# Performance work log

Hardware: AMD Instinct MI355X
Metric: run time of the kernel (lower is better)

Reference implementation:

```python
import jax, jax.numpy as jnp
import numpy as np

B, S, D, H = 2, 2048, 1024, 16
HD = D // H               # head_dim = input_size / num_heads
STEPS = 1                 # update_steps_max extra Hopfield update steps
LN_EPS = 1e-5
SCALING = 1.0 / np.sqrt(HD)  # beta = 1/sqrt(head_dim)


def layernorm(x, g, b):
    m = x.mean(-1, keepdims=True)
    v = ((x - m) ** 2).mean(-1, keepdims=True)
    return (x - m) * jax.lax.rsqrt(v + LN_EPS) * g + b


def setup_inputs() -> dict:
    key = jax.random.key(0)
    ks = jax.random.split(key, 9)
    s = 0.02
    f32 = jnp.float32
    return {
        "data": jax.random.normal(ks[0], (B, S, D), f32),
        # affine LayerNorm params (stored / state / projection patterns)
        "g_k": jnp.ones((D,), f32), "b_k": jnp.zeros((D,), f32),
        "g_q": jnp.ones((D,), f32), "b_q": jnp.zeros((D,), f32),
        "g_v": jnp.ones((D,), f32), "b_v": jnp.zeros((D,), f32),
        # in-projections (q/k/v) and out-projection of HopfieldCore
        "Wq": jax.random.normal(ks[1], (D, D), f32) * s, "bq": jnp.zeros((D,), f32),
        "Wk": jax.random.normal(ks[2], (D, D), f32) * s, "bk": jnp.zeros((D,), f32),
        "Wv": jax.random.normal(ks[3], (D, D), f32) * s, "bv": jnp.zeros((D,), f32),
        "Wo": jax.random.normal(ks[4], (D, D), f32) * s, "bo": jnp.zeros((D,), f32),
    }


def reference(data, g_k, b_k, g_q, b_q, g_v, b_v,
              Wq, bq, Wk, bk, Wv, bv, Wo, bo):
    # single input tensor used as stored / state / projection pattern
    xk = layernorm(data, g_k, b_k)   # stored pattern  -> keys
    xq = layernorm(data, g_q, b_q)   # state pattern   -> queries
    xv = layernorm(data, g_v, b_v)   # pattern proj    -> values

    split = lambda t: t.reshape(B, S, H, HD).transpose(0, 2, 1, 3)  # [B,H,S,HD]
    q = split(xq @ Wq + bq)
    k = split(xk @ Wk + bk)
    v = split(xv @ Wv + bv)

    def assoc(q):  # xi = softmax(beta * q K^T)
        return jax.nn.softmax(
            jnp.einsum('bhqd,bhkd->bhqk', q, k) * SCALING, axis=-1)

    xi = assoc(q)
    for _ in range(STEPS):           # iterative Hopfield update: q <- xi K
        q = jnp.einsum('bhqk,bhkd->bhqd', xi, k)
        xi = assoc(q)

    out = jnp.einsum('bhqk,bhkd->bhqd', xi, v)        # retrieve with values
    out = out.transpose(0, 2, 1, 3).reshape(B, S, D)  # merge heads
    return out @ Wo + bo
```

## Files before the change

kernel.cpp:

```cpp
#include <hip/hip_runtime.h>
#include <hip/hip_bf16.h>

#define B_  2
#define S_  2048
#define D_  1024
#define H_  16
#define HD_ 64
#define M_  4096


typedef __attribute__((ext_vector_type(8))) short short8;
typedef __attribute__((ext_vector_type(4))) float f32x4;

#define CE_ 0.1803368801111204f
#define SD_ 56

static __device__ __forceinline__ unsigned short f2bfc(float f){
  union{float f; unsigned u;} c; c.f = f;
  return (unsigned short)((c.u + 0x8000u) >> 16);
}
static __device__ __forceinline__ unsigned pk2bf(float a, float b){
  union{float f; unsigned u;} ca, cb; ca.f=a; cb.f=b;
  return __builtin_amdgcn_perm(cb.u + 0x8000u, ca.u + 0x8000u, 0x07060302u);
}
static __device__ __forceinline__ unsigned pk2bft(float a, float b){
  union{float f; unsigned u;} ca, cb; ca.f=a; cb.f=b;
  return __builtin_amdgcn_perm(cb.u, ca.u, 0x07060302u);
}

__global__ __launch_bounds__(256) void stats_kernel(const float* __restrict__ x,
                                                    float* __restrict__ mean,
                                                    float* __restrict__ rstd){
  int row = blockIdx.x*4 + (threadIdx.x>>6);
  int l = threadIdx.x & 63;
  const float4* xr = (const float4*)(x + (size_t)row*D_);
  float s = 0.f, ss = 0.f;
  #pragma unroll
  for (int i=0;i<4;i++){
    float4 v = xr[l + 64*i];
    s  += v.x+v.y+v.z+v.w;
    ss += v.x*v.x+v.y*v.y+v.z*v.z+v.w*v.w;
  }
  #pragma unroll
  for (int m=1;m<64;m<<=1){ s += __shfl_xor(s, m, 64); ss += __shfl_xor(ss, m, 64); }
  if (l==0){
    float me = s*(1.0f/D_);
    float var = ss*(1.0f/D_) - me*me;
    mean[row] = me;
    rstd[row] = rsqrtf(var + 1e-5f);
  }
}

__global__ __launch_bounds__(256) void biasfold_kernel(
  const float* __restrict__ Wq, const float* __restrict__ Wk, const float* __restrict__ Wv,
  const float* __restrict__ blq, const float* __restrict__ blk, const float* __restrict__ blv,
  const float* __restrict__ bpq, const float* __restrict__ bpk, const float* __restrict__ bpv,
  float* __restrict__ bf){
  int z = blockIdx.y;
  const float* W  = (z==0)?Wq:(z==1)?Wk:Wv;
  const float* bl = (z==0)?blq:(z==1)?blk:blv;
  const float* bp = (z==0)?bpq:(z==1)?bpk:bpv;
  int nl = threadIdx.x & 63, kg = threadIdx.x >> 6;
  int n = blockIdx.x*64 + nl;
  float acc = 0.f;
  for (int k = kg*256; k < (kg+1)*256; k++)
    acc += bl[k] * W[(size_t)k*D_ + n];
  __shared__ float red[4][64];
  red[kg][nl] = acc;
  __syncthreads();
  if (threadIdx.x < 64){
    int nn = blockIdx.x*64 + threadIdx.x;
    float v = red[0][threadIdx.x]+red[1][threadIdx.x]+red[2][threadIdx.x]+red[3][threadIdx.x]
              + bp[nn];
    bf[z*D_ + nn] = (z==0) ? v*CE_ : v;
  }
}

__global__ __launch_bounds__(256) void wtrans_kernel(
  const float* __restrict__ Wq, const float* __restrict__ Wk,
  const float* __restrict__ Wv, const float* __restrict__ Wo,
  const float* __restrict__ gq, const float* __restrict__ gk,
  const float* __restrict__ gv,
  unsigned short* __restrict__ WT){
  int z = blockIdx.z;
  const float* W = (z==0)?Wq:(z==1)?Wk:(z==2)?Wv:Wo;
  const float* g = (z==0)?gq:(z==1)?gk:(z==2)?gv:(const float*)0;
  unsigned short* out = WT + ((size_t)z<<20);
  int k0 = blockIdx.x*64, n0 = blockIdx.y*64;
  __shared__ unsigned short tile[64][72];
  int t = threadIdx.x;
  {
    int kr = t>>2, c16 = (t&3)*16;
    float gs = g ? g[k0+kr]*((z==0)?CE_:1.0f) : 1.0f;
    const float* src = W + (size_t)(k0+kr)*D_ + n0 + c16;
    float4 w0 = *(const float4*)(src);
    float4 w1 = *(const float4*)(src+4);
    float4 w2 = *(const float4*)(src+8);
    float4 w3 = *(const float4*)(src+12);
    unsigned* tp = (unsigned*)&tile[kr][c16];
    tp[0]=pk2bf(w0.x*gs,w0.y*gs); tp[1]=pk2bf(w0.z*gs,w0.w*gs);
    tp[2]=pk2bf(w1.x*gs,w1.y*gs); tp[3]=pk2bf(w1.z*gs,w1.w*gs);
    tp[4]=pk2bf(w2.x*gs,w2.y*gs); tp[5]=pk2bf(w2.z*gs,w2.w*gs);
    tp[6]=pk2bf(w3.x*gs,w3.y*gs); tp[7]=pk2bf(w3.z*gs,w3.w*gs);
  }
  __syncthreads();
  {
    int nr = t>>2, kc = (t&3)*16;
    union { uint4 v[2]; unsigned short u[16]; } st;
    #pragma unroll
    for (int i=0;i<16;i++) st.u[i] = tile[kc+i][nr];
    unsigned short* dst = out + (size_t)(n0+nr)*D_ + k0 + kc;
    *(uint4*)(dst)     = st.v[0];
    *(uint4*)(dst + 8) = st.v[1];
  }
}

__global__ __launch_bounds__(256) void gemm_qkv(
  const float* __restrict__ data,
  const unsigned short* __restrict__ WT,
  const float* __restrict__ biasf,
  const float* __restrict__ mean, const float* __restrict__ rstd,
  unsigned short* __restrict__ qv, unsigned short* __restrict__ kb,
  unsigned short* __restrict__ kT, unsigned short* __restrict__ vT)
{
  int z = blockIdx.z;
  const unsigned short* Bt = WT + ((size_t)z<<20);
  const float* bias = biasf + z*D_;
  unsigned short* oN = (z==0)?qv:(z==1)?kb:(unsigned short*)0;
  unsigned short* oT = (z==0)?(unsigned short*)0:(z==1)?kT:vT;

  __shared__ __align__(16) unsigned short As[128*SD_];
  __shared__ __align__(16) unsigned short Bs[128*SD_];
  int tid = threadIdx.x, w = tid>>6, l = tid&63;
  int m0 = blockIdx.x*128, n0 = blockIdx.y*128;
  int wr = (w>>1)*64, wc = (w&1)*64;
  int lr = l&15, qd = l>>4;
  int srow = tid>>2, scol = (tid&3)*8;

  float rs0 = rstd[m0+srow],    nm0 = -mean[m0+srow]*rs0;
  float rs1 = rstd[m0+srow+64], nm1 = -mean[m0+srow+64]*rs1;

  const f32x4 fz = {0.f,0.f,0.f,0.f};
  f32x4 acc[4][4];
  #pragma unroll
  for (int i=0;i<4;i++)
    #pragma unroll
    for (int j=0;j<4;j++) acc[i][j] = fz;

  for (int kk=0; kk<D_; kk+=32){
    __syncthreads();
    {
      const float* p0 = data + (size_t)(m0+srow   )*D_ + kk + scol;
      const float* p1 = data + (size_t)(m0+srow+64)*D_ + kk + scol;
      float4 a0 = *(const float4*)(p0), a0b = *(const float4*)(p0+4);
      float4 a1 = *(const float4*)(p1), a1b = *(const float4*)(p1+4);
      uint4 o0, o1;
      o0.x = pk2bf(fmaf(a0.x ,rs0,nm0), fmaf(a0.y ,rs0,nm0));
      o0.y = pk2bf(fmaf(a0.z ,rs0,nm0), fmaf(a0.w ,rs0,nm0));
      o0.z = pk2bf(fmaf(a0b.x,rs0,nm0), fmaf(a0b.y,rs0,nm0));
      o0.w = pk2bf(fmaf(a0b.z,rs0,nm0), fmaf(a0b.w,rs0,nm0));
      o1.x = pk2bf(fmaf(a1.x ,rs1,nm1), fmaf(a1.y ,rs1,nm1));
      o1.y = pk2bf(fmaf(a1.z ,rs1,nm1), fmaf(a1.w ,rs1,nm1));
      o1.z = pk2bf(fmaf(a1b.x,rs1,nm1), fmaf(a1b.y,rs1,nm1));
      o1.w = pk2bf(fmaf(a1b.z,rs1,nm1), fmaf(a1b.w,rs1,nm1));
      *(uint4*)(As + srow*SD_      + scol) = o0;
      *(uint4*)(As + (srow+64)*SD_ + scol) = o1;
    }
    *(uint4*)(Bs + srow*SD_      + scol) = *(const uint4*)(Bt + (size_t)(n0+srow   )*D_ + kk + scol);
    *(uint4*)(Bs + (srow+64)*SD_ + scol) = *(const uint4*)(Bt + (size_t)(n0+srow+64)*D_ + kk + scol);
    __syncthreads();
    short8 af[4], bfr[4];
    #pragma unroll
    for (int i=0;i<4;i++) af[i]  = *(const short8*)(As + (wr + i*16 + lr)*SD_ + qd*8);
    #pragma unroll
    for (int j=0;j<4;j++) bfr[j] = *(const short8*)(Bs + (wc + j*16 + lr)*SD_ + qd*8);
    #pragma unroll
    for (int i=0;i<4;i++)
      #pragma unroll
      for (int j=0;j<4;j++)
        acc[i][j] = __builtin_amdgcn_mfma_f32_16x16x32_bf16(af[i], bfr[j], acc[i][j], 0, 0, 0);
  }

  #pragma unroll
  for (int j=0;j<4;j++){
    int n = n0 + wc + j*16 + lr;
    float bias_n = bias[n];
    #pragma unroll
    for (int i=0;i<4;i++){
      int mb = m0 + wr + i*16 + qd*4;
      float v0 = acc[i][j][0] + bias_n;
      float v1 = acc[i][j][1] + bias_n;
      float v2 = acc[i][j][2] + bias_n;
      float v3 = acc[i][j][3] + bias_n;
      if (oN){
        oN[(size_t)(mb+0)*D_ + n] = f2bfc(v0);
        oN[(size_t)(mb+1)*D_ + n] = f2bfc(v1);
        oN[(size_t)(mb+2)*D_ + n] = f2bfc(v2);
        oN[(size_t)(mb+3)*D_ + n] = f2bfc(v3);
      }
      if (oT){
        int bb = mb >> 11, sI = mb & (S_-1);
        int hh = n >> 6,  dd = n & 63;
        uint2 pk; pk.x = pk2bf(v0, v1); pk.y = pk2bf(v2, v3);
        *(uint2*)(oT + (size_t)((bb*H_ + hh)*HD_ + dd)*S_ + sI) = pk;
      }
    }
  }
}

__global__ __launch_bounds__(256) void gemm_out(
  const unsigned short* __restrict__ A,
  const unsigned short* __restrict__ Bt,
  const float* __restrict__ bo,
  float* __restrict__ Cf)
{
  __shared__ __align__(16) unsigned short As[128*SD_];
  __shared__ __align__(16) unsigned short Bs[128*SD_];
  int tid = threadIdx.x, w = tid>>6, l = tid&63;
  int m0 = blockIdx.x*128, n0 = blockIdx.y*128;
  int wr = (w>>1)*64, wc = (w&1)*64;
  int lr = l&15, qd = l>>4;
  int srow = tid>>2, scol = (tid&3)*8;

  const f32x4 fz = {0.f,0.f,0.f,0.f};
  f32x4 acc[4][4];
  #pragma unroll
  for (int i=0;i<4;i++)
    #pragma unroll
    for (int j=0;j<4;j++) acc[i][j] = fz;

  for (int kk=0; kk<D_; kk+=32){
    __syncthreads();
    *(uint4*)(As + srow*SD_      + scol) = *(const uint4*)(A  + (size_t)(m0+srow   )*D_ + kk + scol);
    *(uint4*)(As + (srow+64)*SD_ + scol) = *(const uint4*)(A  + (size_t)(m0+srow+64)*D_ + kk + scol);
    *(uint4*)(Bs + srow*SD_      + scol) = *(const uint4*)(Bt + (size_t)(n0+srow   )*D_ + kk + scol);
    *(uint4*)(Bs + (srow+64)*SD_ + scol) = *(const uint4*)(Bt + (size_t)(n0+srow+64)*D_ + kk + scol);
    __syncthreads();
    short8 af[4], bfr[4];
    #pragma unroll
    for (int i=0;i<4;i++) af[i]  = *(const short8*)(As + (wr + i*16 + lr)*SD_ + qd*8);
    #pragma unroll
    for (int j=0;j<4;j++) bfr[j] = *(const short8*)(Bs + (wc + j*16 + lr)*SD_ + qd*8);
    #pragma unroll
    for (int i=0;i<4;i++)
      #pragma unroll
      for (int j=0;j<4;j++)
        acc[i][j] = __builtin_amdgcn_mfma_f32_16x16x32_bf16(af[i], bfr[j], acc[i][j], 0, 0, 0);
  }

  #pragma unroll
  for (int j=0;j<4;j++){
    int n = n0 + wc + j*16 + lr;
    float bias_n = bo[n];
    #pragma unroll
    for (int i=0;i<4;i++){
      int mb = m0 + wr + i*16 + qd*4;
      Cf[(size_t)(mb+0)*D_ + n] = acc[i][j][0] + bias_n;
      Cf[(size_t)(mb+1)*D_ + n] = acc[i][j][1] + bias_n;
      Cf[(size_t)(mb+2)*D_ + n] = acc[i][j][2] + bias_n;
      Cf[(size_t)(mb+3)*D_ + n] = acc[i][j][3] + bias_n;
    }
  }
}

__global__ __launch_bounds__(256) void attn_fused(
  unsigned short* __restrict__ QO,
  const unsigned short* __restrict__ K,
  const unsigned short* __restrict__ KT,
  const unsigned short* __restrict__ VT)
{
  int qt = blockIdx.x;
  int h  = blockIdx.y;
  int b  = qt >> 4;
  int bh = b*H_ + h;
  int tid = threadIdx.x, w = tid>>6, l = tid&63;
  int lr = l&15, qd = l>>4;
  int r8 = tid>>3, c8 = (tid&7)*8;
  int chf = c8>>5, co = c8&31;

  __shared__ __align__(16) unsigned short sK[2][64*SD_];
  __shared__ __align__(16) unsigned short sV[2][64*SD_];
  __shared__ __align__(16) unsigned short sP[4][2][32*SD_];

  const f32x4 fz = {0.f,0.f,0.f,0.f};

  unsigned short* Qbase = QO + (size_t)(qt*128 + w*32) * D_ + h*64;
  short8 qf[2][2];
  #pragma unroll
  for (int gg=0; gg<2; gg++)
    #pragma unroll
    for (int hf=0; hf<2; hf++)
      qf[gg][hf] = *(const short8*)(Qbase + (size_t)(gg*16+lr)*D_ + hf*32 + qd*8);

  const unsigned short* Khead = K + (size_t)(b*S_)*D_ + h*64;
  const unsigned short* Vh0 = KT + (size_t)bh*HD_*S_;
  const unsigned short* Vh1 = VT + (size_t)bh*HD_*S_;
  unsigned short* Pw0 = &sP[w][0][0];
  unsigned short* Pw1 = &sP[w][1][0];

  f32x4 oacc[2][4];
  float lac[2];

  uint4 kr0, kr1, vr0, vr1;
  {
    kr0 = *(const uint4*)(Khead + (size_t)(r8   )*D_ + c8);
    kr1 = *(const uint4*)(Khead + (size_t)(r8+32)*D_ + c8);
    vr0 = *(const uint4*)(Vh0 + (size_t)(r8   )*S_ + c8);
    vr1 = *(const uint4*)(Vh0 + (size_t)(r8+32)*S_ + c8);
  }

  #pragma unroll 1
  for (int phase=0; phase<2; phase++){
    const unsigned short* Vhead = phase ? Vh1 : Vh0;
    lac[0]=0.f; lac[1]=0.f;
    #pragma unroll
    for (int gg=0;gg<2;gg++)
      #pragma unroll
      for (int t=0;t<4;t++) oacc[gg][t]=fz;

    for (int kt=0; kt<S_; kt+=64){
      __syncthreads();
      *(uint4*)(&sK[chf][(r8   )*SD_ + co]) = kr0;
      *(uint4*)(&sK[chf][(r8+32)*SD_ + co]) = kr1;
      *(uint4*)(&sV[chf][(r8   )*SD_ + co]) = vr0;
      *(uint4*)(&sV[chf][(r8+32)*SD_ + co]) = vr1;
      __syncthreads();

      {
        int nkt = kt + 64;
        const unsigned short* Vn = Vhead;
        if (nkt >= S_){ nkt = 0; Vn = Vh1; }
        kr0 = *(const uint4*)(Khead + (size_t)(nkt+r8   )*D_ + c8);
        kr1 = *(const uint4*)(Khead + (size_t)(nkt+r8+32)*D_ + c8);
        vr0 = *(const uint4*)(Vn + (size_t)(r8   )*S_ + nkt + c8);
        vr1 = *(const uint4*)(Vn + (size_t)(r8+32)*S_ + nkt + c8);
      }

      f32x4 sc[2][4];
      #pragma unroll
      for (int st=0; st<4; st++){
        short8 kA0 = *(const short8*)(&sK[0][(st*16+lr)*SD_ + qd*8]);
        short8 kA1 = *(const short8*)(&sK[1][(st*16+lr)*SD_ + qd*8]);
        #pragma unroll
        for (int gg=0; gg<2; gg++){
          f32x4 z = fz;
          z = __builtin_amdgcn_mfma_f32_16x16x32_bf16(kA0, qf[gg][0], z, 0,0,0);
          z = __builtin_amdgcn_mfma_f32_16x16x32_bf16(kA1, qf[gg][1], z, 0,0,0);
          sc[gg][st] = z;
        }
      }
      #pragma unroll
      for (int gg=0; gg<2; gg++)
        #pragma unroll
        for (int st=0; st<4; st++){
          float p0=__builtin_amdgcn_exp2f(sc[gg][st][0]);
          float p1=__builtin_amdgcn_exp2f(sc[gg][st][1]);
          float p2=__builtin_amdgcn_exp2f(sc[gg][st][2]);
          float p3=__builtin_amdgcn_exp2f(sc[gg][st][3]);
          lac[gg] += (p0+p1)+(p2+p3);
          uint2 pk; pk.x = pk2bft(p0,p1); pk.y = pk2bft(p2,p3);
          unsigned short* Ph = (st&2) ? Pw1 : Pw0;
          *(uint2*)(Ph + (gg*16+lr)*SD_ + (st&1)*16 + qd*4) = pk;
        }
      short8 pf[2][2];
      #pragma unroll
      for (int gg=0; gg<2; gg++){
        pf[gg][0] = *(const short8*)(Pw0 + (gg*16+lr)*SD_ + qd*8);
        pf[gg][1] = *(const short8*)(Pw1 + (gg*16+lr)*SD_ + qd*8);
      }
      #pragma unroll
      for (int dt=0; dt<4; dt++){
        short8 vA0 = *(const short8*)(&sV[0][(dt*16+lr)*SD_ + qd*8]);
        short8 vA1 = *(const short8*)(&sV[1][(dt*16+lr)*SD_ + qd*8]);
        #pragma unroll
        for (int gg=0; gg<2; gg++){
          oacc[gg][dt] = __builtin_amdgcn_mfma_f32_16x16x32_bf16(vA0, pf[gg][0], oacc[gg][dt], 0,0,0);
          oacc[gg][dt] = __builtin_amdgcn_mfma_f32_16x16x32_bf16(vA1, pf[gg][1], oacc[gg][dt], 0,0,0);
        }
      }
    }

    #pragma unroll
    for (int gg=0;gg<2;gg++){
      lac[gg] += __shfl_xor(lac[gg], 16, 64);
      lac[gg] += __shfl_xor(lac[gg], 32, 64);
    }

    if (phase==0){
      #pragma unroll
      for (int gg=0;gg<2;gg++){
        float iv = CE_ * __builtin_amdgcn_rcpf(lac[gg]);
        #pragma unroll
        for (int dt=0;dt<4;dt++){
          uint2 pk;
          pk.x = pk2bf(oacc[gg][dt][0]*iv, oacc[gg][dt][1]*iv);
          pk.y = pk2bf(oacc[gg][dt][2]*iv, oacc[gg][dt][3]*iv);
          unsigned short* Ph = (dt&2) ? Pw1 : Pw0;
          *(uint2*)(Ph + (gg*16+lr)*SD_ + (dt&1)*16 + qd*4) = pk;
        }
      }
      __builtin_amdgcn_s_waitcnt(0);
      #pragma unroll
      for (int gg=0;gg<2;gg++){
        qf[gg][0] = *(const short8*)(Pw0 + (gg*16+lr)*SD_ + qd*8);
        qf[gg][1] = *(const short8*)(Pw1 + (gg*16+lr)*SD_ + qd*8);
      }
    } else {
      #pragma unroll
      for (int gg=0;gg<2;gg++){
        float iv = __builtin_amdgcn_rcpf(lac[gg]);
        unsigned short* Ob = QO + (size_t)(qt*128 + w*32 + gg*16 + lr)*D_ + h*64;
        #pragma unroll
        for (int dt=0;dt<4;dt++){
          uint2 pk;
          pk.x = pk2bf(oacc[gg][dt][0]*iv, oacc[gg][dt][1]*iv);
          pk.y = pk2bf(oacc[gg][dt][2]*iv, oacc[gg][dt][3]*iv);
          *(uint2*)(Ob + dt*16 + qd*4) = pk;
        }
      }
    }
  }
}

extern "C" void kernel_launch(void* const* d_in, const int* in_sizes, int n_in,
                              void* d_out, int out_size, void* d_ws, size_t ws_size,
                              hipStream_t stream){
  const float* data = (const float*)d_in[0];
  const float* g_k  = (const float*)d_in[1];
  const float* b_k  = (const float*)d_in[2];
  const float* g_q  = (const float*)d_in[3];
  const float* b_q  = (const float*)d_in[4];
  const float* g_v  = (const float*)d_in[5];
  const float* b_v  = (const float*)d_in[6];
  const float* Wq   = (const float*)d_in[7];
  const float* bq   = (const float*)d_in[8];
  const float* Wk   = (const float*)d_in[9];
  const float* bk   = (const float*)d_in[10];
  const float* Wv   = (const float*)d_in[11];
  const float* bv   = (const float*)d_in[12];
  const float* Wo   = (const float*)d_in[13];
  const float* bo   = (const float*)d_in[14];
  float* out = (float*)d_out;

  char* ws = (char*)d_ws;
  const size_t MB = (size_t)1<<20;
  unsigned short* q    = (unsigned short*)(ws);
  unsigned short* kb   = (unsigned short*)(ws + 8*MB);
  unsigned short* WT   = (unsigned short*)(ws + 16*MB);
  unsigned short* WTo  = WT + ((size_t)3<<20);
  float*          bfld = (float*)(ws + 24*MB);
  float*          mean = bfld + 3*D_;
  float*          rstd = mean + M_;
  unsigned short* vT   = (unsigned short*)d_out;
  unsigned short* kT   = (unsigned short*)((char*)d_out + 8*MB);

  dim3 gb(256);
  stats_kernel<<<dim3(M_/4), gb, 0, stream>>>(data, mean, rstd);
  biasfold_kernel<<<dim3(16,3), gb, 0, stream>>>(Wq,Wk,Wv, b_q,b_k,b_v, bq,bk,bv, bfld);
  wtrans_kernel<<<dim3(16,16,4), gb, 0, stream>>>(Wq,Wk,Wv,Wo, g_q,g_k,g_v, WT);
  gemm_qkv<<<dim3(32,8,3), gb, 0, stream>>>(data, WT, bfld, mean, rstd, q, kb, kT, vT);
  attn_fused<<<dim3(32, H_), gb, 0, stream>>>(q, kb, kT, vT);
  gemm_out<<<dim3(32,8), gb, 0, stream>>>(q, WTo, bo, out);
}
```

Measured before the change: 292.4 us.

## Merge prep kernels, use direct global-to-LDS loads, widen attention key tiles

Folds the stats, bias-fold and weight-transpose kernels into one prep launch to cut launch overhead. Both GEMMs now stage their bf16 operand tiles with global_load_lds directly into unpadded LDS rows, skipping the register round trip. The attention kernel processes 128-key tiles in two 64-key sub-steps. It computes the softmax row sums with an MFMA against a ones vector instead of scalar adds plus cross-lane shuffles. The unpadded LDS rows risk bank conflicts, and the per-wave P buffer shrinks to 16 rows and is reused across query groups, which relies on in-order LDS access.

```diff
diff --git a/kernel.cpp b/kernel.cpp
--- a/kernel.cpp
+++ b/kernel.cpp
@@ -15,6 +15,12 @@
 #define CE_ 0.1803368801111204f
 #define SD_ 56
 
+typedef __attribute__((address_space(1))) const unsigned GU;
+typedef __attribute__((address_space(3))) unsigned LU;
+static __device__ __forceinline__ void glds16(const void* g, void* l){
+  __builtin_amdgcn_global_load_lds((GU*)g, (LU*)l, 16, 0, 0);
+}
+
 static __device__ __forceinline__ unsigned short f2bfc(float f){
   union{float f; unsigned u;} c; c.f = f;
   return (unsigned short)((c.u + 0x8000u) >> 16);
@@ -28,90 +34,86 @@
   return __builtin_amdgcn_perm(cb.u, ca.u, 0x07060302u);
 }
 
-__global__ __launch_bounds__(256) void stats_kernel(const float* __restrict__ x,
-                                                    float* __restrict__ mean,
-                                                    float* __restrict__ rstd){
-  int row = blockIdx.x*4 + (threadIdx.x>>6);
-  int l = threadIdx.x & 63;
-  const float4* xr = (const float4*)(x + (size_t)row*D_);
-  float s = 0.f, ss = 0.f;
-  #pragma unroll
-  for (int i=0;i<4;i++){
-    float4 v = xr[l + 64*i];
-    s  += v.x+v.y+v.z+v.w;
-    ss += v.x*v.x+v.y*v.y+v.z*v.z+v.w*v.w;
-  }
-  #pragma unroll
-  for (int m=1;m<64;m<<=1){ s += __shfl_xor(s, m, 64); ss += __shfl_xor(ss, m, 64); }
-  if (l==0){
-    float me = s*(1.0f/D_);
-    float var = ss*(1.0f/D_) - me*me;
-    mean[row] = me;
-    rstd[row] = rsqrtf(var + 1e-5f);
-  }
-}
-
-__global__ __launch_bounds__(256) void biasfold_kernel(
-  const float* __restrict__ Wq, const float* __restrict__ Wk, const float* __restrict__ Wv,
+__global__ __launch_bounds__(256) void prep_kernel(
+  const float* __restrict__ data, float* __restrict__ mean, float* __restrict__ rstd,
+  const float* __restrict__ Wq, const float* __restrict__ Wk,
+  const float* __restrict__ Wv, const float* __restrict__ Wo,
+  const float* __restrict__ gq, const float* __restrict__ gk, const float* __restrict__ gv,
   const float* __restrict__ blq, const float* __restrict__ blk, const float* __restrict__ blv,
   const float* __restrict__ bpq, const float* __restrict__ bpk, const float* __restrict__ bpv,
-  float* __restrict__ bf){
-  int z = blockIdx.y;
-  const float* W  = (z==0)?Wq:(z==1)?Wk:Wv;
-  const float* bl = (z==0)?blq:(z==1)?blk:blv;
-  const float* bp = (z==0)?bpq:(z==1)?bpk:bpv;
-  int nl = threadIdx.x & 63, kg = threadIdx.x >> 6;
-  int n = blockIdx.x*64 + nl;
-  float acc = 0.f;
-  for (int k = kg*256; k < (kg+1)*256; k++)
-    acc += bl[k] * W[(size_t)k*D_ + n];
+  unsigned short* __restrict__ WT, float* __restrict__ bf)
+{
+  __shared__ unsigned short tile[64][72];
   __shared__ float red[4][64];
-  red[kg][nl] = acc;
-  __syncthreads();
-  if (threadIdx.x < 64){
-    int nn = blockIdx.x*64 + threadIdx.x;
-    float v = red[0][threadIdx.x]+red[1][threadIdx.x]+red[2][threadIdx.x]+red[3][threadIdx.x]
-              + bp[nn];
-    bf[z*D_ + nn] = (z==0) ? v*CE_ : v;
-  }
-}
-
-__global__ __launch_bounds__(256) void wtrans_kernel(
-  const float* __restrict__ Wq, const float* __restrict__ Wk,
-  const float* __restrict__ Wv, const float* __restrict__ Wo,
-  const float* __restrict__ gq, const float* __restrict__ gk,
-  const float* __restrict__ gv,
-  unsigned short* __restrict__ WT){
-  int z = blockIdx.z;
-  const float* W = (z==0)?Wq:(z==1)?Wk:(z==2)?Wv:Wo;
-  const float* g = (z==0)?gq:(z==1)?gk:(z==2)?gv:(const float*)0;
-  unsigned short* out = WT + ((size_t)z<<20);
-  int k0 = blockIdx.x*64, n0 = blockIdx.y*64;
-  __shared__ unsigned short tile[64][72];
-  int t = threadIdx.x;
-  {
-    int kr = t>>2, c16 = (t&3)*16;
-    float gs = g ? g[k0+kr]*((z==0)?CE_:1.0f) : 1.0f;
-    const float* src = W + (size_t)(k0+kr)*D_ + n0 + c16;
-    float4 w0 = *(const float4*)(src);
-    float4 w1 = *(const float4*)(src+4);
-    float4 w2 = *(const float4*)(src+8);
-    float4 w3 = *(const float4*)(src+12);
-    unsigned* tp = (unsigned*)&tile[kr][c16];
-    tp[0]=pk2bf(w0.x*gs,w0.y*gs); tp[1]=pk2bf(w0.z*gs,w0.w*gs);
-    tp[2]=pk2bf(w1.x*gs,w1.y*gs); tp[3]=pk2bf(w1.z*gs,w1.w*gs);
-    tp[4]=pk2bf(w2.x*gs,w2.y*gs); tp[5]=pk2bf(w2.z*gs,w2.w*gs);
-    tp[6]=pk2bf(w3.x*gs,w3.y*gs); tp[7]=pk2bf(w3.z*gs,w3.w*gs);
-  }
-  __syncthreads();
-  {
-    int nr = t>>2, kc = (t&3)*16;
-    union { uint4 v[2]; unsigned short u[16]; } st;
-    #pragma unroll
-    for (int i=0;i<16;i++) st.u[i] = tile[kc+i][nr];
-    unsigned short* dst = out + (size_t)(n0+nr)*D_ + k0 + kc;
-    *(uint4*)(dst)     = st.v[0];
-    *(uint4*)(dst + 8) = st.v[1];
+  int bid = blockIdx.x, t = threadIdx.x;
+  if (bid < 1024){
+    int row = bid*4 + (t>>6);
+    int l = t & 63;
+    const float4* xr = (const float4*)(data + (size_t)row*D_);
+    float s = 0.f, ss = 0.f;
+    #pragma unroll
+    for (int i=0;i<4;i++){
+      float4 v = xr[l + 64*i];
+      s  += v.x+v.y+v.z+v.w;
+      ss += v.x*v.x+v.y*v.y+v.z*v.z+v.w*v.w;
+    }
+    #pragma unroll
+    for (int m=1;m<64;m<<=1){ s += __shfl_xor(s, m, 64); ss += __shfl_xor(ss, m, 64); }
+    if (l==0){
+      float me = s*(1.0f/D_);
+      float var = ss*(1.0f/D_) - me*me;
+      mean[row] = me;
+      rstd[row] = rsqrtf(var + 1e-5f);
+    }
+  } else if (bid < 2048){
+    int idx = bid - 1024;
+    int z = idx >> 8, rem = idx & 255;
+    int k0 = (rem>>4)*64, n0 = (rem&15)*64;
+    const float* W = (z==0)?Wq:(z==1)?Wk:(z==2)?Wv:Wo;
+    const float* g = (z==0)?gq:(z==1)?gk:(z==2)?gv:(const float*)0;
+    unsigned short* out = WT + ((size_t)z<<20);
+    {
+      int kr = t>>2, c16 = (t&3)*16;
+      float gs = g ? g[k0+kr]*((z==0)?CE_:1.0f) : 1.0f;
+      const float* src = W + (size_t)(k0+kr)*D_ + n0 + c16;
+      float4 w0 = *(const float4*)(src);
+      float4 w1 = *(const float4*)(src+4);
+      float4 w2 = *(const float4*)(src+8);
+      float4 w3 = *(const float4*)(src+12);
+      unsigned* tp = (unsigned*)&tile[kr][c16];
+      tp[0]=pk2bf(w0.x*gs,w0.y*gs); tp[1]=pk2bf(w0.z*gs,w0.w*gs);
+      tp[2]=pk2bf(w1.x*gs,w1.y*gs); tp[3]=pk2bf(w1.z*gs,w1.w*gs);
+      tp[4]=pk2bf(w2.x*gs,w2.y*gs); tp[5]=pk2bf(w2.z*gs,w2.w*gs);
+      tp[6]=pk2bf(w3.x*gs,w3.y*gs); tp[7]=pk2bf(w3.z*gs,w3.w*gs);
+    }
+    __syncthreads();
+    {
+      int nr = t>>2, kc = (t&3)*16;
+      union { uint4 v[2]; unsigned short u[16]; } st;
+      #pragma unroll
+      for (int i=0;i<16;i++) st.u[i] = tile[kc+i][nr];
+      unsigned short* dst = out + (size_t)(n0+nr)*D_ + k0 + kc;
+      *(uint4*)(dst)     = st.v[0];
+      *(uint4*)(dst + 8) = st.v[1];
+    }
+  } else {
+    int idx = bid - 2048;
+    int z = idx >> 4, xb = idx & 15;
+    const float* W  = (z==0)?Wq:(z==1)?Wk:Wv;
+    const float* bl = (z==0)?blq:(z==1)?blk:blv;
+    const float* bp = (z==0)?bpq:(z==1)?bpk:bpv;
+    int nl = t & 63, kg = t >> 6;
+    int n = xb*64 + nl;
+    float acc = 0.f;
+    for (int k = kg*256; k < (kg+1)*256; k++)
+      acc += bl[k] * W[(size_t)k*D_ + n];
+    red[kg][nl] = acc;
+    __syncthreads();
+    if (t < 64){
+      int nn = xb*64 + t;
+      float v = red[0][t]+red[1][t]+red[2][t]+red[3][t] + bp[nn];
+      bf[z*D_ + nn] = (z==0) ? v*CE_ : v;
+    }
   }
 }
 
@@ -130,7 +132,7 @@
   unsigned short* oT = (z==0)?(unsigned short*)0:(z==1)?kT:vT;
 
   __shared__ __align__(16) unsigned short As[128*SD_];
-  __shared__ __align__(16) unsigned short Bs[128*SD_];
+  __shared__ __align__(16) unsigned short Bs[128*32];
   int tid = threadIdx.x, w = tid>>6, l = tid&63;
   int m0 = blockIdx.x*128, n0 = blockIdx.y*128;
   int wr = (w>>1)*64, wc = (w&1)*64;
@@ -140,6 +142,10 @@
   float rs0 = rstd[m0+srow],    nm0 = -mean[m0+srow]*rs0;
   float rs1 = rstd[m0+srow+64], nm1 = -mean[m0+srow+64]*rs1;
 
+  const unsigned short* gB = Bt + (size_t)(n0 + w*32 + (l>>2))*D_ + (l&3)*8;
+  unsigned short* lB0 = &Bs[(w*32)*32];
+  unsigned short* lB1 = &Bs[(w*32+16)*32];
+
   const f32x4 fz = {0.f,0.f,0.f,0.f};
   f32x4 acc[4][4];
   #pragma unroll
@@ -149,6 +155,8 @@
 
   for (int kk=0; kk<D_; kk+=32){
     __syncthreads();
+    glds16(gB + kk,                lB0);
+    glds16(gB + kk + (size_t)16*D_, lB1);
     {
       const float* p0 = data + (size_t)(m0+srow   )*D_ + kk + scol;
       const float* p1 = data + (size_t)(m0+srow+64)*D_ + kk + scol;
@@ -166,14 +174,12 @@
       *(uint4*)(As + srow*SD_      + scol) = o0;
       *(uint4*)(As + (srow+64)*SD_ + scol) = o1;
     }
-    *(uint4*)(Bs + srow*SD_      + scol) = *(const uint4*)(Bt + (size_t)(n0+srow   )*D_ + kk + scol);
-    *(uint4*)(Bs + (srow+64)*SD_ + scol) = *(const uint4*)(Bt + (size_t)(n0+srow+64)*D_ + kk + scol);
     __syncthreads();
     short8 af[4], bfr[4];
     #pragma unroll
     for (int i=0;i<4;i++) af[i]  = *(const short8*)(As + (wr + i*16 + lr)*SD_ + qd*8);
     #pragma unroll
-    for (int j=0;j<4;j++) bfr[j] = *(const short8*)(Bs + (wc + j*16 + lr)*SD_ + qd*8);
+    for (int j=0;j<4;j++) bfr[j] = *(const short8*)(Bs + (wc + j*16 + lr)*32 + qd*8);
     #pragma unroll
     for (int i=0;i<4;i++)
       #pragma unroll
@@ -214,13 +220,19 @@
   const float* __restrict__ bo,
   float* __restrict__ Cf)
 {
-  __shared__ __align__(16) unsigned short As[128*SD_];
-  __shared__ __align__(16) unsigned short Bs[128*SD_];
+  __shared__ __align__(16) unsigned short As[128*32];
+  __shared__ __align__(16) unsigned short Bs[128*32];
   int tid = threadIdx.x, w = tid>>6, l = tid&63;
   int m0 = blockIdx.x*128, n0 = blockIdx.y*128;
   int wr = (w>>1)*64, wc = (w&1)*64;
   int lr = l&15, qd = l>>4;
-  int srow = tid>>2, scol = (tid&3)*8;
+
+  const unsigned short* gA = A  + (size_t)(m0 + w*32 + (l>>2))*D_ + (l&3)*8;
+  const unsigned short* gB = Bt + (size_t)(n0 + w*32 + (l>>2))*D_ + (l&3)*8;
+  unsigned short* lA0 = &As[(w*32)*32];
+  unsigned short* lA1 = &As[(w*32+16)*32];
+  unsigned short* lB0 = &Bs[(w*32)*32];
+  unsigned short* lB1 = &Bs[(w*32+16)*32];
 
   const f32x4 fz = {0.f,0.f,0.f,0.f};
   f32x4 acc[4][4];
@@ -231,16 +243,16 @@
 
   for (int kk=0; kk<D_; kk+=32){
     __syncthreads();
-    *(uint4*)(As + srow*SD_      + scol) = *(const uint4*)(A  + (size_t)(m0+srow   )*D_ + kk + scol);
-    *(uint4*)(As + (srow+64)*SD_ + scol) = *(const uint4*)(A  + (size_t)(m0+srow+64)*D_ + kk + scol);
-    *(uint4*)(Bs + srow*SD_      + scol) = *(const uint4*)(Bt + (size_t)(n0+srow   )*D_ + kk + scol);
-    *(uint4*)(Bs + (srow+64)*SD_ + scol) = *(const uint4*)(Bt + (size_t)(n0+srow+64)*D_ + kk + scol);
+    glds16(gA + kk,                 lA0);
+    glds16(gA + kk + (size_t)16*D_, lA1);
+    glds16(gB + kk,                 lB0);
+    glds16(gB + kk + (size_t)16*D_, lB1);
     __syncthreads();
     short8 af[4], bfr[4];
     #pragma unroll
-    for (int i=0;i<4;i++) af[i]  = *(const short8*)(As + (wr + i*16 + lr)*SD_ + qd*8);
-    #pragma unroll
-    for (int j=0;j<4;j++) bfr[j] = *(const short8*)(Bs + (wc + j*16 + lr)*SD_ + qd*8);
+    for (int i=0;i<4;i++) af[i]  = *(const short8*)(As + (wr + i*16 + lr)*32 + qd*8);
+    #pragma unroll
+    for (int j=0;j<4;j++) bfr[j] = *(const short8*)(Bs + (wc + j*16 + lr)*32 + qd*8);
     #pragma unroll
     for (int i=0;i<4;i++)
       #pragma unroll
@@ -269,20 +281,20 @@
   const unsigned short* __restrict__ KT,
   const unsigned short* __restrict__ VT)
 {
-  int qt = blockIdx.x;
-  int h  = blockIdx.y;
-  int b  = qt >> 4;
-  int bh = b*H_ + h;
+  int qt = blockIdx.x, h = blockIdx.y;
+  int b = qt >> 4, bh = b*H_ + h;
   int tid = threadIdx.x, w = tid>>6, l = tid&63;
   int lr = l&15, qd = l>>4;
   int r8 = tid>>3, c8 = (tid&7)*8;
   int chf = c8>>5, co = c8&31;
 
-  __shared__ __align__(16) unsigned short sK[2][64*SD_];
-  __shared__ __align__(16) unsigned short sV[2][64*SD_];
-  __shared__ __align__(16) unsigned short sP[4][2][32*SD_];
+  __shared__ __align__(16) unsigned short sK[2][128*SD_];
+  __shared__ __align__(16) unsigned short sV[4][64*SD_];
+  __shared__ __align__(16) unsigned short sP[4][2][16*SD_];
 
   const f32x4 fz = {0.f,0.f,0.f,0.f};
+  const short8 vones = {(short)0x3F80,(short)0x3F80,(short)0x3F80,(short)0x3F80,
+                        (short)0x3F80,(short)0x3F80,(short)0x3F80,(short)0x3F80};
 
   unsigned short* Qbase = QO + (size_t)(qt*128 + w*32) * D_ + h*64;
   short8 qf[2][2];
@@ -298,117 +310,116 @@
   unsigned short* Pw0 = &sP[w][0][0];
   unsigned short* Pw1 = &sP[w][1][0];
 
-  f32x4 oacc[2][4];
-  float lac[2];
-
-  uint4 kr0, kr1, vr0, vr1;
-  {
-    kr0 = *(const uint4*)(Khead + (size_t)(r8   )*D_ + c8);
-    kr1 = *(const uint4*)(Khead + (size_t)(r8+32)*D_ + c8);
-    vr0 = *(const uint4*)(Vh0 + (size_t)(r8   )*S_ + c8);
-    vr1 = *(const uint4*)(Vh0 + (size_t)(r8+32)*S_ + c8);
-  }
+  f32x4 oacc[2][4], sacc[2];
+
+  uint4 kr[4], vr[4];
+  #pragma unroll
+  for (int j=0;j<4;j++)
+    kr[j] = *(const uint4*)(Khead + (size_t)(r8 + j*32)*D_ + c8);
+  vr[0] = *(const uint4*)(Vh0 + (size_t)(r8   )*S_ + c8);
+  vr[1] = *(const uint4*)(Vh0 + (size_t)(r8+32)*S_ + c8);
+  vr[2] = *(const uint4*)(Vh0 + (size_t)(r8   )*S_ + 64 + c8);
+  vr[3] = *(const uint4*)(Vh0 + (size_t)(r8+32)*S_ + 64 + c8);
 
   #pragma unroll 1
   for (int phase=0; phase<2; phase++){
     const unsigned short* Vhead = phase ? Vh1 : Vh0;
-    lac[0]=0.f; lac[1]=0.f;
+    sacc[0]=fz; sacc[1]=fz;
     #pragma unroll
     for (int gg=0;gg<2;gg++)
       #pragma unroll
       for (int t=0;t<4;t++) oacc[gg][t]=fz;
 
-    for (int kt=0; kt<S_; kt+=64){
+    for (int kt=0; kt<S_; kt+=128){
       __syncthreads();
-      *(uint4*)(&sK[chf][(r8   )*SD_ + co]) = kr0;
-      *(uint4*)(&sK[chf][(r8+32)*SD_ + co]) = kr1;
-      *(uint4*)(&sV[chf][(r8   )*SD_ + co]) = vr0;
-      *(uint4*)(&sV[chf][(r8+32)*SD_ + co]) = vr1;
+      #pragma unroll
+      for (int j=0;j<4;j++)
+        *(uint4*)(&sK[chf][(r8 + j*32)*SD_ + co]) = kr[j];
+      *(uint4*)(&sV[chf  ][(r8   )*SD_ + co]) = vr[0];
+      *(uint4*)(&sV[chf  ][(r8+32)*SD_ + co]) = vr[1];
+      *(uint4*)(&sV[chf+2][(r8   )*SD_ + co]) = vr[2];
+      *(uint4*)(&sV[chf+2][(r8+32)*SD_ + co]) = vr[3];
       __syncthreads();
 
       {
-        int nkt = kt + 64;
+        int nkt = kt + 128;
         const unsigned short* Vn = Vhead;
         if (nkt >= S_){ nkt = 0; Vn = Vh1; }
-        kr0 = *(const uint4*)(Khead + (size_t)(nkt+r8   )*D_ + c8);
-        kr1 = *(const uint4*)(Khead + (size_t)(nkt+r8+32)*D_ + c8);
-        vr0 = *(const uint4*)(Vn + (size_t)(r8   )*S_ + nkt + c8);
-        vr1 = *(const uint4*)(Vn + (size_t)(r8+32)*S_ + nkt + c8);
-      }
-
-      f32x4 sc[2][4];
-      #pragma unroll
-      for (int st=0; st<4; st++){
-        short8 kA0 = *(const short8*)(&sK[0][(st*16+lr)*SD_ + qd*8]);
-        short8 kA1 = *(const short8*)(&sK[1][(st*16+lr)*SD_ + qd*8]);
+        #pragma unroll
+        for (int j=0;j<4;j++)
+          kr[j] = *(const uint4*)(Khead + (size_t)(nkt + r8 + j*32)*D_ + c8);
+        vr[0] = *(const uint4*)(Vn + (size_t)(r8   )*S_ + nkt + c8);
+        vr[1] = *(const uint4*)(Vn + (size_t)(r8+32)*S_ + nkt + c8);
+        vr[2] = *(const uint4*)(Vn + (size_t)(r8   )*S_ + nkt + 64 + c8);
+        vr[3] = *(const uint4*)(Vn + (size_t)(r8+32)*S_ + nkt + 64 + c8);
+      }
+
+      #pragma unroll
+      for (int sub=0; sub<2; sub++){
+        int ko = sub<<6;
+        f32x4 sc[2][4];
+        #pragma unroll
+        for (int st=0; st<4; st++){
+          short8 kA0 = *(const short8*)(&sK[0][(ko+st*16+lr)*SD_ + qd*8]);
+          short8 kA1 = *(const short8*)(&sK[1][(ko+st*16+lr)*SD_ + qd*8]);
+          #pragma unroll
+          for (int gg=0; gg<2; gg++){
+            f32x4 zz = fz;
+            zz = __builtin_amdgcn_mfma_f32_16x16x32_bf16(kA0, qf[gg][0], zz, 0,0,0);
+            zz = __builtin_amdgcn_mfma_f32_16x16x32_bf16(kA1, qf[gg][1], zz, 0,0,0);
+            sc[gg][st] = zz;
+          }
+        }
+        short8 pf[2][2];
         #pragma unroll
         for (int gg=0; gg<2; gg++){
-          f32x4 z = fz;
-          z = __builtin_amdgcn_mfma_f32_16x16x32_bf16(kA0, qf[gg][0], z, 0,0,0);
-          z = __builtin_amdgcn_mfma_f32_16x16x32_bf16(kA1, qf[gg][1], z, 0,0,0);
-          sc[gg][st] = z;
+          #pragma unroll
+          for (int st=0; st<4; st++){
+            float p0=__builtin_amdgcn_exp2f(sc[gg][st][0]);
+            float p1=__builtin_amdgcn_exp2f(sc[gg][st][1]);
+            float p2=__builtin_amdgcn_exp2f(sc[gg][st][2]);
+            float p3=__builtin_amdgcn_exp2f(sc[gg][st][3]);
+            uint2 pk; pk.x = pk2bft(p0,p1); pk.y = pk2bft(p2,p3);
+            unsigned short* Ph = (st&2) ? Pw1 : Pw0;
+            *(uint2*)(Ph + lr*SD_ + (st&1)*16 + qd*4) = pk;
+          }
+          pf[gg][0] = *(const short8*)(Pw0 + lr*SD_ + qd*8);
+          pf[gg][1] = *(const short8*)(Pw1 + lr*SD_ + qd*8);
+          sacc[gg] = __builtin_amdgcn_mfma_f32_16x16x32_bf16(vones, pf[gg][0], sacc[gg], 0,0,0);
+          sacc[gg] = __builtin_amdgcn_mfma_f32_16x16x32_bf16(vones, pf[gg][1], sacc[gg], 0,0,0);
         }
-      }
-      #pragma unroll
-      for (int gg=0; gg<2; gg++)
-        #pragma unroll
-        for (int st=0; st<4; st++){
-          float p0=__builtin_amdgcn_exp2f(sc[gg][st][0]);
-          float p1=__builtin_amdgcn_exp2f(sc[gg][st][1]);
-          float p2=__builtin_amdgcn_exp2f(sc[gg][st][2]);
-          float p3=__builtin_amdgcn_exp2f(sc[gg][st][3]);
-          lac[gg] += (p0+p1)+(p2+p3);
-          uint2 pk; pk.x = pk2bft(p0,p1); pk.y = pk2bft(p2,p3);
-          unsigned short* Ph = (st&2) ? Pw1 : Pw0;
-          *(uint2*)(Ph + (gg*16+lr)*SD_ + (st&1)*16 + qd*4) = pk;
+        #pragma unroll
+        for (int dt=0; dt<4; dt++){
+          short8 vA0 = *(const short8*)(&sV[sub*2  ][(dt*16+lr)*SD_ + qd*8]);
+          short8 vA1 = *(const short8*)(&sV[sub*2+1][(dt*16+lr)*SD_ + qd*8]);
+          #pragma unroll
+          for (int gg=0; gg<2; gg++){
+            oacc[gg][dt] = __builtin_amdgcn_mfma_f32_16x16x32_bf16(vA0, pf[gg][0], oacc[gg][dt], 0,0,0);
+            oacc[gg][dt] = __builtin_amdgcn_mfma_f32_16x16x32_bf16(vA1, pf[gg][1], oacc[gg][dt], 0,0,0);
+          }
         }
-      short8 pf[2][2];
-      #pragma unroll
-      for (int gg=0; gg<2; gg++){
-        pf[gg][0] = *(const short8*)(Pw0 + (gg*16+lr)*SD_ + qd*8);
-        pf[gg][1] = *(const short8*)(Pw1 + (gg*16+lr)*SD_ + qd*8);
-      }
-      #pragma unroll
-      for (int dt=0; dt<4; dt++){
-        short8 vA0 = *(const short8*)(&sV[0][(dt*16+lr)*SD_ + qd*8]);
-        short8 vA1 = *(const short8*)(&sV[1][(dt*16+lr)*SD_ + qd*8]);
-        #pragma unroll
-        for (int gg=0; gg<2; gg++){
-          oacc[gg][dt] = __builtin_amdgcn_mfma_f32_16x16x32_bf16(vA0, pf[gg][0], oacc[gg][dt], 0,0,0);
-          oacc[gg][dt] = __builtin_amdgcn_mfma_f32_16x16x32_bf16(vA1, pf[gg][1], oacc[gg][dt], 0,0,0);
-        }
-      }
-    }
-
-    #pragma unroll
-    for (int gg=0;gg<2;gg++){
-      lac[gg] += __shfl_xor(lac[gg], 16, 64);
-      lac[gg] += __shfl_xor(lac[gg], 32, 64);
+      }
     }
 
     if (phase==0){
       #pragma unroll
       for (int gg=0;gg<2;gg++){
-        float iv = CE_ * __builtin_amdgcn_rcpf(lac[gg]);
+        float iv = CE_ * __builtin_amdgcn_rcpf(sacc[gg][0]);
         #pragma unroll
         for (int dt=0;dt<4;dt++){
           uint2 pk;
           pk.x = pk2bf(oacc[gg][dt][0]*iv, oacc[gg][dt][1]*iv);
           pk.y = pk2bf(oacc[gg][dt][2]*iv, oacc[gg][dt][3]*iv);
           unsigned short* Ph = (dt&2) ? Pw1 : Pw0;
-          *(uint2*)(Ph + (gg*16+lr)*SD_ + (dt&1)*16 + qd*4) = pk;
+          *(uint2*)(Ph + lr*SD_ + (dt&1)*16 + qd*4) = pk;
         }
-      }
-      __builtin_amdgcn_s_waitcnt(0);
+        qf[gg][0] = *(const short8*)(Pw0 + lr*SD_ + qd*8);
+        qf[gg][1] = *(const short8*)(Pw1 + lr*SD_ + qd*8);
+      }
+    } else {
       #pragma unroll
       for (int gg=0;gg<2;gg++){
-        qf[gg][0] = *(const short8*)(Pw0 + (gg*16+lr)*SD_ + qd*8);
-        qf[gg][1] = *(const short8*)(Pw1 + (gg*16+lr)*SD_ + qd*8);
-      }
-    } else {
-      #pragma unroll
-      for (int gg=0;gg<2;gg++){
-        float iv = __builtin_amdgcn_rcpf(lac[gg]);
+        float iv = __builtin_amdgcn_rcpf(sacc[gg][0]);
         unsigned short* Ob = QO + (size_t)(qt*128 + w*32 + gg*16 + lr)*D_ + h*64;
         #pragma unroll
         for (int dt=0;dt<4;dt++){
@@ -455,9 +466,9 @@
   unsigned short* kT   = (unsigned short*)((char*)d_out + 8*MB);
 
   dim3 gb(256);
-  stats_kernel<<<dim3(M_/4), gb, 0, stream>>>(data, mean, rstd);
-  biasfold_kernel<<<dim3(16,3), gb, 0, stream>>>(Wq,Wk,Wv, b_q,b_k,b_v, bq,bk,bv, bfld);
-  wtrans_kernel<<<dim3(16,16,4), gb, 0, stream>>>(Wq,Wk,Wv,Wo, g_q,g_k,g_v, WT);
+  prep_kernel<<<dim3(2096), gb, 0, stream>>>(data, mean, rstd,
+                                             Wq, Wk, Wv, Wo, g_q, g_k, g_v,
+                                             b_q, b_k, b_v, bq, bk, bv, WT, bfld);
   gemm_qkv<<<dim3(32,8,3), gb, 0, stream>>>(data, WT, bfld, mean, rstd, q, kb, kT, vT);
   attn_fused<<<dim3(32, H_), gb, 0, stream>>>(q, kb, kT, vT);
   gemm_out<<<dim3(32,8), gb, 0, stream>>>(q, WTo, bo, out);
```

New measurement: 336.9 us. 15.2% more time.
